# Performance work log

Hardware: AMD Instinct MI355X
Metric: run time of the kernel (lower is better)

Reference implementation:

```python
import jax, jax.numpy as jnp
import numpy as np

SIGMA = 1e-4  # BlendParams().sigma default in pytorch3d


def setup_inputs() -> dict:
    key = jax.random.key(0)
    k1, k2, k3, k4 = jax.random.split(key, 4)
    N, H, W, K = 8, 512, 512, 16
    # z-buffer depths (positive in front of camera, arbitrary for background)
    zbuf = jax.random.uniform(k1, (N, H, W, K), jnp.float32, 0.1, 10.0)
    # signed 2D distances pixel-center -> face edge, on the scale of sigma
    dists = jax.random.normal(k2, (N, H, W, K), jnp.float32) * 1e-4
    p2f = jax.random.randint(k3, (N, H, W, K), 0, 20000)
    drop = jax.random.uniform(k4, (N, H, W, K)) < 0.2
    pix_to_face = jnp.where(drop, -1, p2f).astype(jnp.int64)
    return {"zbuf": zbuf, "dists": dists, "pix_to_face": pix_to_face}


def reference(zbuf, dists, pix_to_face):
    # colors = zbuf repeated over 3 channels; blend uses top face only for RGB
    # sigmoid_alpha_blend:
    #   prob  = sigmoid(-dists / sigma) * (pix_to_face >= 0)
    #   alpha = 1 - prod_K (1 - prob)
    #   rgb   = colors[..., 0, :]  (== zbuf[..., 0] broadcast to 3 channels)
    mask = (pix_to_face >= 0).astype(zbuf.dtype)  # [N,H,W,K]
    prob = jax.nn.sigmoid(-dists / SIGMA) * mask  # [N,H,W,K]
    alpha = 1.0 - jnp.prod(1.0 - prob, axis=-1)   # [N,H,W]
    rgb = jnp.broadcast_to(zbuf[..., 0:1], zbuf.shape[:-1] + (3,))  # [N,H,W,3]
    return jnp.concatenate([rgb, alpha[..., None]], axis=-1)  # [N,H,W,4]
```

## Files before the change

### kernel.cpp

```cpp
#include <hip/hip_runtime.h>

#define INV_SIGMA 1.0e4f

__device__ __forceinline__ float one_minus_prob(float d, int f) {
    float s = 1.0f / (1.0f + __expf(-d * INV_SIGMA));
    return (f >= 0) ? s : 1.0f;
}

__global__ __launch_bounds__(256) void SelfShader_9921374454199_kernel(
    const float* __restrict__ zbuf,
    const float* __restrict__ dists,
    const int*   __restrict__ p2f,
    float*       __restrict__ out,
    int P)
{
    int i = blockIdx.x * blockDim.x + threadIdx.x;
    if (i >= P) return;

    size_t base = (size_t)i * 16;

    const float4* d4 = reinterpret_cast<const float4*>(dists + base);
    const int4*   f4 = reinterpret_cast<const int4*>(p2f + base);

    float prod = 1.0f;
#pragma unroll
    for (int j = 0; j < 4; ++j) {
        float4 d = d4[j];
        int4   f = f4[j];
        prod *= one_minus_prob(d.x, f.x);
        prod *= one_minus_prob(d.y, f.y);
        prod *= one_minus_prob(d.z, f.z);
        prod *= one_minus_prob(d.w, f.w);
    }

    float alpha = 1.0f - prod;
    float z = zbuf[base];

    float4 o = make_float4(z, z, z, alpha);
    reinterpret_cast<float4*>(out)[i] = o;
}

extern "C" void kernel_launch(void* const* d_in, const int* in_sizes, int n_in,
                              void* d_out, int out_size, void* d_ws, size_t ws_size,
                              hipStream_t stream) {
    const float* zbuf  = (const float*)d_in[0];
    const float* dists = (const float*)d_in[1];
    const int*   p2f   = (const int*)d_in[2];
    float*       out   = (float*)d_out;

    int P = in_sizes[0] / 16;
    int block = 256;
    int grid  = (P + block - 1) / block;
    SelfShader_9921374454199_kernel<<<grid, block, 0, stream>>>(zbuf, dists, p2f, out, P);
}
```

Measured before the change: 355.8 us.

## Split each pixel across four lanes with coalesced loads and shuffle reduction

Each pixel's 16 K-values are now spread over 4 consecutive threads, so neighbouring lanes load adjacent float4 chunks of dists and pix_to_face instead of striding 64 bytes apart. The per-pixel product is combined with two xor shuffles within each 4-lane group. Each lane then writes one scalar of the RGBA output, and each block handles 1024 chunks across 4 iterations. This trades one vector store per pixel for four scalar stores plus shuffles, and every lane now touches its zbuf chunk, although only the first lane's value is used.

```diff
diff --git a/kernel.cpp b/kernel.cpp
--- a/kernel.cpp
+++ b/kernel.cpp
@@ -12,32 +12,35 @@
     const float* __restrict__ dists,
     const int*   __restrict__ p2f,
     float*       __restrict__ out,
-    int P)
+    long long nChunks)
 {
-    int i = blockIdx.x * blockDim.x + threadIdx.x;
-    if (i >= P) return;
+    const float4* d4 = reinterpret_cast<const float4*>(dists);
+    const int4*   f4 = reinterpret_cast<const int4*>(p2f);
+    const float4* z4 = reinterpret_cast<const float4*>(zbuf);
 
-    size_t base = (size_t)i * 16;
+    int t = threadIdx.x;
+    int j = t & 3;
+    long long cbase = (long long)blockIdx.x * 1024 + t;
 
-    const float4* d4 = reinterpret_cast<const float4*>(dists + base);
-    const int4*   f4 = reinterpret_cast<const int4*>(p2f + base);
+#pragma unroll
+    for (int r = 0; r < 4; ++r) {
+        long long c = cbase + r * 256;
+        if (c >= nChunks) break;
 
-    float prod = 1.0f;
-#pragma unroll
-    for (int j = 0; j < 4; ++j) {
-        float4 d = d4[j];
-        int4   f = f4[j];
-        prod *= one_minus_prob(d.x, f.x);
-        prod *= one_minus_prob(d.y, f.y);
-        prod *= one_minus_prob(d.z, f.z);
-        prod *= one_minus_prob(d.w, f.w);
+        float4 d = d4[c];
+        int4   f = f4[c];
+        float  z = z4[c].x;
+
+        float prod = one_minus_prob(d.x, f.x) * one_minus_prob(d.y, f.y) *
+                     one_minus_prob(d.z, f.z) * one_minus_prob(d.w, f.w);
+
+        prod *= __shfl_xor(prod, 1, 4);
+        prod *= __shfl_xor(prod, 2, 4);
+
+        float zz = __shfl(z, 0, 4);
+
+        out[c] = (j == 3) ? (1.0f - prod) : zz;
     }
-
-    float alpha = 1.0f - prod;
-    float z = zbuf[base];
-
-    float4 o = make_float4(z, z, z, alpha);
-    reinterpret_cast<float4*>(out)[i] = o;
 }
 
 extern "C" void kernel_launch(void* const* d_in, const int* in_sizes, int n_in,
@@ -48,8 +51,9 @@
     const int*   p2f   = (const int*)d_in[2];
     float*       out   = (float*)d_out;
 
-    int P = in_sizes[0] / 16;
-    int block = 256;
-    int grid  = (P + block - 1) / block;
-    SelfShader_9921374454199_kernel<<<grid, block, 0, stream>>>(zbuf, dists, p2f, out, P);
+    long long nChunks = (long long)in_sizes[0] / 4;
+    int  block = 256;
+    long long chunksPerBlock = 1024;
+    int  grid = (int)((nChunks + chunksPerBlock - 1) / chunksPerBlock);
+    SelfShader_9921374454199_kernel<<<grid, block, 0, stream>>>(zbuf, dists, p2f, out, nChunks);
 }
```

New measurement: 361.0 us. Within noise of the previous version (+1.5%).
